# Kernel tuning notes

Hardware: AMD Instinct MI355X
Metric: run time of the kernel (lower is better)

## Reference

```python
import jax, jax.numpy as jnp
import numpy as np

# Tensor layout: x is [b, c, d, h, w, p, q, r] = [batch, channels, D, H, W, pd, ph, pw]
LETTERS = 'bcdhwpqr'

def axial_linear(x, W, b, axis, S, C):
    """LinearAlongDims1 over dims [1, axis]: jointly mixes channels and one
    spatial/patch axis. Torch flattens in (spatial, channel) order, so the
    (S*C, S*C) weight is reshaped to [S_out, C_out, S_in, C_in]."""
    a = LETTERS[axis]
    W4 = W.reshape(S, C, S, C)
    out_sub = LETTERS.replace('c', 'Y').replace(a, 'X')
    y = jnp.einsum(f'{LETTERS},XY{a}c->{out_sub}', x, W4)
    bshape = [1] * 8
    bshape[1] = C
    bshape[axis] = S
    return y + b.reshape(S, C).T.reshape(bshape)


def _make_linear_params(key, n):
    kw, kb = jax.random.split(key)
    bound = 1.0 / np.sqrt(n)
    W = jax.random.uniform(kw, (n, n), jnp.float32, -bound, bound)
    b = jax.random.uniform(kb, (n,), jnp.float32, -bound, bound)
    return W, b


def setup_inputs() -> dict:
    key = jax.random.key(0)
    ks = jax.random.split(key, 7)
    B, C, D, P = 2, 64, 16, 4
    x = jax.random.normal(ks[0], (B, C, D, D, D, P, P, P), jnp.float32)
    w_d, b_d = _make_linear_params(ks[1], C * D)      # image_d: dims [1,2]
    w_h, b_h = _make_linear_params(ks[2], C * D)      # image_h: dims [1,3]
    w_w, b_w = _make_linear_params(ks[3], C * D)      # image_w: dims [1,4]
    w_pd, b_pd = _make_linear_params(ks[4], C * P)    # patch_d: dims [1,5]
    w_ph, b_ph = _make_linear_params(ks[5], C * P)    # patch_h: dims [1,6]
    w_pw, b_pw = _make_linear_params(ks[6], C * P)    # patch_w: dims [1,7]
    return {
        'x': x,
        'w_d': w_d, 'b_d': b_d, 'w_h': w_h, 'b_h': b_h, 'w_w': w_w, 'b_w': b_w,
        'w_pd': w_pd, 'b_pd': b_pd, 'w_ph': w_ph, 'b_ph': b_ph,
        'w_pw': w_pw, 'b_pw': b_pw,
    }


def reference(x, w_d, b_d, w_h, b_h, w_w, b_w,
              w_pd, b_pd, w_ph, b_ph, w_pw, b_pw):
    C = x.shape[1]
    D = x.shape[2]
    P = x.shape[5]
    y = axial_linear(x, w_pd, b_pd, 5, P, C)
    y = y + axial_linear(x, w_ph, b_ph, 6, P, C)
    y = y + axial_linear(x, w_pw, b_pw, 7, P, C)
    y = y + axial_linear(x, w_d, b_d, 2, D, C)
    y = y + axial_linear(x, w_h, b_h, 3, D, C)
    y = y + axial_linear(x, w_w, b_w, 4, D, C)
    # shapes match -> leaky_relu + residual (module returns y; gn(x) is discarded)
    y = x + jax.nn.leaky_relu(y, negative_slope=0.01)
    return y
```

## Files before the change

### kernel.cpp

```cpp
#include <hip/hip_runtime.h>

typedef __attribute__((ext_vector_type(8))) short short8;
typedef __attribute__((ext_vector_type(4))) float floatx4;


__device__ __forceinline__ unsigned short f2bf(float f){
  unsigned int u = __float_as_uint(f);
  u += 0x7FFFu + ((u >> 16) & 1u);
  return (unsigned short)(u >> 16);
}

template<int AX>
__device__ __forceinline__ int tidx(int m, int a, int c){
  if      (AX==0){ int b=m>>14, t=m&16383;                         return (b<<24)|(c<<18)|(a<<14)|t; }
  else if (AX==1){ int b=m>>14, d=(m>>10)&15, t=m&1023;            return (b<<24)|(c<<18)|(d<<14)|(a<<10)|t; }
  else           { int b=m>>14, d=(m>>10)&15, h=(m>>6)&15, t=m&63; return (b<<24)|(c<<18)|(d<<14)|(h<<10)|(a<<6)|t; }
}

template<int AX>
__device__ __forceinline__ int srcbase(int m){
  if      (AX==0) return ((m>>14)<<24) | (((m>>10)&15)<<16) | (((m>>6)&15)<<12) | ((m&63)<<6);
  else if (AX==1) return ((m>>14)<<24) | (((m>>10)&15)<<20) | (((m>>6)&15)<<12) | ((m&63)<<6);
  else            return ((m>>14)<<24) | (((m>>10)&15)<<20) | (((m>>6)&15)<<16) | ((m&63)<<6);
}

#define ASYNC_CP16(g, l) \
  __builtin_amdgcn_global_load_lds( \
      (const __attribute__((address_space(1))) unsigned int*)(g), \
      (__attribute__((address_space(3))) unsigned int*)(l), 16, 0, 0)

__global__ __launch_bounds__(256) void castw_all(
    const float* __restrict__ wa, const float* __restrict__ wb, const float* __restrict__ wc,
    const float* __restrict__ wd_, const float* __restrict__ we, const float* __restrict__ wf,
    const float* __restrict__ bd_, const float* __restrict__ bh_, const float* __restrict__ bw_,
    const float* __restrict__ bpd_, const float* __restrict__ bph_, const float* __restrict__ bpw_,
    unsigned short* oa, unsigned short* ob, unsigned short* oc,
    unsigned short* od, unsigned short* oe, unsigned short* of_,
    float* __restrict__ Bimg, float* __restrict__ Bpat){
  int blk = blockIdx.x;
  if (blk < 6528){
    const float* src; unsigned short* dst; int idx;
    if (blk < 6144){ int wsel = blk >> 11, loc = blk & 2047;
      src = wsel==0?wa:(wsel==1?wb:wc); dst = wsel==0?oa:(wsel==1?ob:oc);
      idx = loc*256 + threadIdx.x; }
    else { int b2 = blk - 6144, wsel = b2 >> 7, loc = b2 & 127;
      src = wsel==0?wd_:(wsel==1?we:wf); dst = wsel==0?od:(wsel==1?oe:of_);
      idx = loc*256 + threadIdx.x; }
    float2 v = ((const float2*)src)[idx];
    ((unsigned int*)dst)[idx] = (unsigned int)f2bf(v.x) | ((unsigned int)f2bf(v.y) << 16);
  } else if (blk < 7552){
    int idx = (blk - 6528)*256 + threadIdx.x;
    int c = idx & 63, wv = (idx>>6)&15, hv = (idx>>10)&15, dv = idx>>14;
    Bimg[idx] = bd_[dv*64+c] + bh_[hv*64+c] + bw_[wv*64+c];
  } else {
    int idx = (blk - 7552)*256 + threadIdx.x;
    int c = idx & 63, tt = idx>>6;
    int p = tt>>4, q = (tt>>2)&3, r = tt&3;
    Bpat[idx] = bpd_[p*64+c] + bph_[q*64+c] + bpw_[r*64+c];
  }
}

__global__ __launch_bounds__(256) void transpose_cx(const float* __restrict__ x,
                                                    unsigned short* __restrict__ xt){
  __shared__ float T[64][65];
  int b  = blockIdx.x >> 12;
  int s0 = (blockIdx.x & 4095) * 64;
  int t = threadIdx.x;
  int cr = t >> 4, sq = t & 15;
  #pragma unroll
  for (int it = 0; it < 4; it++){
    int c = it*16 + cr;
    float4 v = *(const float4*)(x + (b<<24) + (c<<18) + s0 + sq*4);
    T[c][sq*4+0]=v.x; T[c][sq*4+1]=v.y; T[c][sq*4+2]=v.z; T[c][sq*4+3]=v.w;
  }
  __syncthreads();
  int sw = t >> 2, cq = t & 3;
  unsigned int pk[8];
  #pragma unroll
  for (int i=0;i<8;i++){
    float f0 = T[cq*16 + 2*i    ][sw];
    float f1 = T[cq*16 + 2*i + 1][sw];
    pk[i] = (unsigned int)f2bf(f0) | ((unsigned int)f2bf(f1) << 16);
  }
  uint4* dst = (uint4*)(xt + (b<<24) + ((s0 + sw)<<6) + cq*16);
  dst[0] = make_uint4(pk[0],pk[1],pk[2],pk[3]);
  dst[1] = make_uint4(pk[4],pk[5],pk[6],pk[7]);
}

template<int AXI, bool FIRST>
__device__ __forceinline__ void patch_axis(const unsigned short* Xs,
                                           const unsigned short* __restrict__ W,
                                           float* AccL, int w, int l16, int q8){
  floatx4 acc[4][2];
  #pragma unroll
  for (int nt=0;nt<4;nt++)
    #pragma unroll
    for (int mt=0;mt<2;mt++) acc[nt][mt] = (floatx4){0.f,0.f,0.f,0.f};

  #pragma unroll 2
  for (int kit = 0; kit < 8; kit++){
    int a = kit >> 1;
    short8 bf[2], af[4];
    int u = (AXI==0) ? (a*16 + l16)
          : (AXI==1) ? ((l16>>2)*16 + a*4 + (l16&3))
                     : ((l16>>2)*16 + (l16&3)*4 + a);
    int jg = ((kit & 1) << 2) + q8;
    #pragma unroll
    for (int mt = 0; mt < 2; mt++){
      int r = mt*64 + u;
      int j = jg ^ ((r ^ (r >> 3)) & 7);
      bf[mt] = *(const short8*)(Xs + r*64 + j*8);
    }
    #pragma unroll
    for (int nt = 0; nt < 4; nt++){
      int n = w*64 + nt*16 + l16;
      af[nt] = *(const short8*)(W + n*256 + kit*32 + q8*8);
    }
    #pragma unroll
    for (int nt=0; nt<4; nt++)
      #pragma unroll
      for (int mt=0; mt<2; mt++)
        acc[nt][mt] = __builtin_amdgcn_mfma_f32_16x16x32_bf16(af[nt], bf[mt], acc[nt][mt], 0,0,0);
  }

  int uo = (AXI==0) ? (w*16 + l16)
         : (AXI==1) ? ((l16>>2)*16 + w*4 + (l16&3))
                    : ((l16>>2)*16 + (l16&3)*4 + w);
  #pragma unroll
  for (int nt=0; nt<4; nt++)
    #pragma unroll
    for (int mt=0; mt<2; mt++){
      float* p = AccL + (mt*64 + uo)*65 + nt*16 + q8*4;
      #pragma unroll
      for (int rg=0; rg<4; rg++){
        if (FIRST) p[rg]  = acc[nt][mt][rg];
        else       p[rg] += acc[nt][mt][rg];
      }
    }
}

__global__ __launch_bounds__(256) void patch_fused(const unsigned short* __restrict__ xt,
    const unsigned short* __restrict__ Wp_, const unsigned short* __restrict__ Wq_,
    const unsigned short* __restrict__ Wr_, float* __restrict__ out){
  __shared__ float AccL[2*64*65];
  __shared__ unsigned short Xs[8192];
  int pp = blockIdx.x;
  int b = pp >> 11, dpair = pp & 2047;
  const unsigned short* xp = xt + (b<<24) + dpair*8192;
  int t = threadIdx.x, w = t>>6, lane = t&63, q8 = lane>>4, l16 = lane&15;

  #pragma unroll
  for (int i = 0; i < 4; i++){
    int L = i*256 + t;
    int r = L >> 3, jl = L & 7;
    int jg = jl ^ ((r ^ (r >> 3)) & 7);
    ASYNC_CP16(xp + r*64 + jg*8, Xs + i*2048 + w*512);
  }
  __syncthreads();

  patch_axis<0,true >(Xs, Wp_, AccL, w, l16, q8);
  __syncthreads();
  patch_axis<1,false>(Xs, Wq_, AccL, w, l16, q8);
  __syncthreads();
  patch_axis<2,false>(Xs, Wr_, AccL, w, l16, q8);
  __syncthreads();

  int sbase = dpair*128;
  #pragma unroll
  for (int it = 0; it < 32; it++){
    int lin = it*256 + t;
    int c = lin >> 7, rem = lin & 127, pt = rem >> 6, u = rem & 63;
    out[(b<<24) | (c<<18) | (sbase + pt*64 + u)] = AccL[(pt*64+u)*65 + c];
  }
}

template<int AX, int EPI>
__global__ __launch_bounds__(256) void gemm_img(const unsigned short* __restrict__ xt,
                                                const unsigned short* __restrict__ Wbf,
                                                float* __restrict__ out,
                                                const float* __restrict__ x,
                                                const float* __restrict__ Bimg,
                                                const float* __restrict__ Bpat){
  constexpr int K  = 1024;
  constexpr int SA = (AX==0)?(1<<20):(AX==1)?(1<<16):(1<<12);
  int B = blockIdx.x;
  int xcd = B & 7, seq = B >> 3;
  int nt = seq & 7;
  int mt = (seq >> 3) * 8 + xcd;

  __shared__ unsigned short Xs[128*64];
  __shared__ unsigned short Ws[128*64];

  int t = threadIdx.x, lane = t & 63, wid = t >> 6;
  int wn = (wid & 1) << 6, wm = (wid >> 1) << 6;
  int q8 = lane >> 4, l16 = lane & 15;

  floatx4 acc[4][4];
  #pragma unroll
  for (int i=0;i<4;i++)
    #pragma unroll
    for (int j=0;j<4;j++) acc[i][j] = (floatx4){0.f,0.f,0.f,0.f};

  const unsigned short* Wp = Wbf + (size_t)nt*128*K;

  int rr = t >> 3;
  int jg = (t & 7) ^ ((t >> 3) & 7);
  int baseX[4], baseWo[4];
  #pragma unroll
  for (int c=0;c<4;c++){
    int r = c*32 + rr;
    baseX[c]  = srcbase<AX>(mt*128 + r) + jg*8;
    baseWo[c] = r*K + jg*8;
  }

  int xoff[4], woff[4];
  #pragma unroll
  for (int i=0;i<4;i++){
    int rx = wm + i*16 + l16; xoff[i] = rx*64 + ((q8 ^ (rx & 7)) << 3);
    int rw = wn + i*16 + l16; woff[i] = rw*64 + ((q8 ^ (rw & 7)) << 3);
  }

  for (int a = 0; a < 16; a++){
    #pragma unroll
    for (int c=0;c<4;c++){
      ASYNC_CP16(xt + baseX[c] + a*SA, Xs + c*2048 + wid*512);
      ASYNC_CP16(Wp + baseWo[c] + a*64, Ws + c*2048 + wid*512);
    }
    __syncthreads();

    #pragma unroll
    for (int kk=0; kk<2; kk++){
      short8 wf[4], xf[4];
      #pragma unroll
      for (int i=0;i<4;i++){
        wf[i] = *(const short8*)&Ws[woff[i] ^ (kk<<5)];
        xf[i] = *(const short8*)&Xs[xoff[i] ^ (kk<<5)];
      }
      #pragma unroll
      for (int i=0;i<4;i++)
        #pragma unroll
        for (int j=0;j<4;j++)
          acc[i][j] = __builtin_amdgcn_mfma_f32_16x16x32_bf16(wf[i], xf[j], acc[i][j], 0,0,0);
    }
    __syncthreads();
  }

  #pragma unroll
  for (int i=0;i<4;i++){
    #pragma unroll
    for (int j=0;j<4;j++){
      int mg = mt*128 + wm + j*16 + l16;
      if (EPI){
        int d = (mg>>10)&15, h = (mg>>6)&15, tt = mg&63;
        int n0 = nt*128 + wn + i*16 + q8*4;
        int a = n0 >> 6, c0 = n0 & 63;
        float4 bi = *(const float4*)(Bimg + (((d*16 + h)*16 + a)*64 + c0));
        float4 bp = *(const float4*)(Bpat + (tt*64 + c0));
        float bs0 = bi.x + bp.x, bs1 = bi.y + bp.y, bs2 = bi.z + bp.z, bs3 = bi.w + bp.w;
        #pragma unroll
        for (int rg=0; rg<4; rg++){
          int ng = n0 + rg;
          int idx = tidx<AX>(mg, ng>>6, ng&63);
          float bsum = (rg==0)?bs0:(rg==1)?bs1:(rg==2)?bs2:bs3;
          float y = out[idx] + acc[i][j][rg] + bsum;
          out[idx] = x[idx] + (y >= 0.f ? y : 0.01f*y);
        }
      } else {
        #pragma unroll
        for (int rg=0; rg<4; rg++){
          int ng = nt*128 + wn + i*16 + q8*4 + rg;
          int idx = tidx<AX>(mg, ng>>6, ng&63);
          out[idx] += acc[i][j][rg];
        }
      }
    }
  }
}

extern "C" void kernel_launch(void* const* d_in, const int* in_sizes, int n_in,
                              void* d_out, int out_size, void* d_ws, size_t ws_size,
                              hipStream_t stream){
  const float* x = (const float*)d_in[0];
  const float* Wsrc[6] = {(const float*)d_in[1], (const float*)d_in[3], (const float*)d_in[5],
                          (const float*)d_in[7], (const float*)d_in[9], (const float*)d_in[11]};
  const float* Bsrc[6] = {(const float*)d_in[2], (const float*)d_in[4], (const float*)d_in[6],
                          (const float*)d_in[8], (const float*)d_in[10], (const float*)d_in[12]};
  float* out = (float*)d_out;
  char* ws = (char*)d_ws;

  const size_t welems[6] = {1024u*1024u, 1024u*1024u, 1024u*1024u,
                            256u*256u, 256u*256u, 256u*256u};
  size_t wOff[6], o = 0;
  for (int i=0;i<6;i++){ wOff[i] = o; o += welems[i]*2; }
  size_t xtOff = (o + 255) & ~(size_t)255;
  size_t bimgOff = xtOff + ((size_t)1u<<25)*2;
  size_t bpatOff = bimgOff + (size_t)16*16*16*64*4;
  unsigned short* xt = (unsigned short*)(ws + xtOff);
  float* Bimg = (float*)(ws + bimgOff);
  float* Bpat = (float*)(ws + bpatOff);
  unsigned short* Wbf[6];
  for (int i=0;i<6;i++) Wbf[i] = (unsigned short*)(ws + wOff[i]);

  castw_all<<<7616,256,0,stream>>>(Wsrc[0],Wsrc[1],Wsrc[2],Wsrc[3],Wsrc[4],Wsrc[5],
                                   Bsrc[0],Bsrc[1],Bsrc[2],Bsrc[3],Bsrc[4],Bsrc[5],
                                   Wbf[0],Wbf[1],Wbf[2],Wbf[3],Wbf[4],Wbf[5],
                                   Bimg, Bpat);
  transpose_cx<<<8192,256,0,stream>>>(x, xt);

  patch_fused<<<4096,256,0,stream>>>(xt, Wbf[3], Wbf[4], Wbf[5], out);

  gemm_img<0,0><<<2048,256,0,stream>>>(xt, Wbf[0], out, nullptr, nullptr, nullptr);
  gemm_img<1,0><<<2048,256,0,stream>>>(xt, Wbf[1], out, nullptr, nullptr, nullptr);
  gemm_img<2,1><<<2048,256,0,stream>>>(xt, Wbf[2], out, x, Bimg, Bpat);
}
```

Before: 852.7 us.

## Double-buffer LDS tiles in image-axis GEMM with explicit vmcnt waits

The K loop of the image-axis GEMM now uses two LDS buffers, so the async global-to-LDS copy of the next tile is issued while the current tile is consumed by MFMAs. Synchronisation uses raw s_barrier and partial s_waitcnt vmcnt counts instead of __syncthreads. The block-to-tile mapping also drops the XCD-aware swizzle in favour of a plain mt/nt split. LDS use doubles, which may lower occupancy, and the hand-counted vmcnt waits depend on exactly eight copies per stage.

New measurement: 848.5 us. Within noise of the previous version (-0.5%).

```diff
diff --git a/kernel.cpp b/kernel.cpp
--- a/kernel.cpp
+++ b/kernel.cpp
@@ -174,6 +174,9 @@
   }
 }
 
+#define WAITV8 asm volatile("s_waitcnt vmcnt(8)" ::: "memory")
+#define WAITV0 asm volatile("s_waitcnt vmcnt(0)" ::: "memory")
+
 template<int AX, int EPI>
 __global__ __launch_bounds__(256) void gemm_img(const unsigned short* __restrict__ xt,
                                                 const unsigned short* __restrict__ Wbf,
@@ -183,13 +186,11 @@
                                                 const float* __restrict__ Bpat){
   constexpr int K  = 1024;
   constexpr int SA = (AX==0)?(1<<20):(AX==1)?(1<<16):(1<<12);
-  int B = blockIdx.x;
-  int xcd = B & 7, seq = B >> 3;
-  int nt = seq & 7;
-  int mt = (seq >> 3) * 8 + xcd;
-
-  __shared__ unsigned short Xs[128*64];
-  __shared__ unsigned short Ws[128*64];
+  int Bk = blockIdx.x;
+  int mt = Bk >> 3, nt = Bk & 7;
+
+  __shared__ unsigned short Xs0[128*64], Ws0[128*64];
+  __shared__ unsigned short Xs1[128*64], Ws1[128*64];
 
   int t = threadIdx.x, lane = t & 63, wid = t >> 6;
   int wn = (wid & 1) << 6, wm = (wid >> 1) << 6;
@@ -220,30 +221,50 @@
     int rw = wn + i*16 + l16; woff[i] = rw*64 + ((q8 ^ (rw & 7)) << 3);
   }
 
-  for (int a = 0; a < 16; a++){
-    #pragma unroll
-    for (int c=0;c<4;c++){
-      ASYNC_CP16(xt + baseX[c] + a*SA, Xs + c*2048 + wid*512);
-      ASYNC_CP16(Wp + baseWo[c] + a*64, Ws + c*2048 + wid*512);
-    }
-    __syncthreads();
-
-    #pragma unroll
-    for (int kk=0; kk<2; kk++){
-      short8 wf[4], xf[4];
-      #pragma unroll
-      for (int i=0;i<4;i++){
-        wf[i] = *(const short8*)&Ws[woff[i] ^ (kk<<5)];
-        xf[i] = *(const short8*)&Xs[xoff[i] ^ (kk<<5)];
-      }
-      #pragma unroll
-      for (int i=0;i<4;i++)
-        #pragma unroll
-        for (int j=0;j<4;j++)
-          acc[i][j] = __builtin_amdgcn_mfma_f32_16x16x32_bf16(wf[i], xf[j], acc[i][j], 0,0,0);
-    }
-    __syncthreads();
-  }
+  #define STAGE_T(a, XS, WS) do { \
+    _Pragma("unroll") \
+    for (int c=0;c<4;c++){ \
+      ASYNC_CP16(xt + baseX[c] + (a)*SA, (XS) + c*2048 + wid*512); \
+      ASYNC_CP16(Wp + baseWo[c] + (a)*64, (WS) + c*2048 + wid*512); \
+    } } while(0)
+
+  #define COMPUTE_T(XS, WS) do { \
+    _Pragma("unroll") \
+    for (int kk=0; kk<2; kk++){ \
+      short8 wf[4], xf[4]; \
+      _Pragma("unroll") \
+      for (int i=0;i<4;i++){ \
+        wf[i] = *(const short8*)&(WS)[woff[i] ^ (kk<<5)]; \
+        xf[i] = *(const short8*)&(XS)[xoff[i] ^ (kk<<5)]; \
+      } \
+      _Pragma("unroll") \
+      for (int i=0;i<4;i++) \
+        _Pragma("unroll") \
+        for (int j=0;j<4;j++) \
+          acc[i][j] = __builtin_amdgcn_mfma_f32_16x16x32_bf16(wf[i], xf[j], acc[i][j], 0,0,0); \
+    } } while(0)
+
+  STAGE_T(0, Xs0, Ws0);
+  WAITV0;
+  __builtin_amdgcn_s_barrier();
+  STAGE_T(1, Xs1, Ws1);
+
+  for (int a2 = 0; a2 < 8; a2++){
+    COMPUTE_T(Xs0, Ws0);
+    __builtin_amdgcn_s_barrier();
+    if (a2 < 7){ STAGE_T(2*a2+2, Xs0, Ws0); WAITV8; }
+    else       { WAITV0; }
+    __builtin_amdgcn_s_barrier();
+    COMPUTE_T(Xs1, Ws1);
+    if (a2 < 7){
+      __builtin_amdgcn_s_barrier();
+      STAGE_T(2*a2+3, Xs1, Ws1);
+      WAITV8;
+      __builtin_amdgcn_s_barrier();
+    }
+  }
+  #undef STAGE_T
+  #undef COMPUTE_T
 
   #pragma unroll
   for (int i=0;i<4;i++){
```
